# Kernel optimization log

Hardware: AMD Instinct MI355X
Metric: run time of the kernel (lower is better)

Reference implementation:

```python
import jax, jax.numpy as jnp
import numpy as np

B, S, H = 2, 2048, 1024
NUM_HEAD = 16
HEAD = H // NUM_HEAD
NEG = -10000000000.0


def setup_inputs() -> dict:
    key = jax.random.key(0)
    ks = jax.random.split(key, 10)
    scale = 1.0 / np.sqrt(H)
    return {
        "query": jax.random.normal(ks[0], (B, S, H), jnp.float32),
        "key": jax.random.normal(ks[1], (B, S, H), jnp.float32),
        "value": jax.random.normal(ks[2], (B, S, H), jnp.float32),
        "mask": jax.random.randint(ks[3], (B, S), 0, 2, jnp.int32),
        "Wq": jax.random.normal(ks[4], (H, H), jnp.float32) * scale,
        "bq": jnp.zeros((H,), jnp.float32),
        "Wk": jax.random.normal(ks[5], (H, H), jnp.float32) * scale,
        "bk": jnp.zeros((H,), jnp.float32),
        "Wv": jax.random.normal(ks[6], (H, H), jnp.float32) * scale,
        "bv": jnp.zeros((H,), jnp.float32),
    }


def reference(query, key, value, mask, Wq, bq, Wk, bk, Wv, bv):
    b, s, h = query.shape
    # Linear projections (torch Linear: x @ W.T + b), split into heads -> [b, nh, s, hd]
    def proj(x, W, bias):
        y = x @ W.T + bias
        return y.reshape(b, s, NUM_HEAD, HEAD).transpose(0, 2, 1, 3)

    q = proj(query, Wq, bq)
    k = proj(key, Wk, bk)
    v = proj(value, Wv, bv)

    # NOTE: original module has NO 1/sqrt(head_dim) scaling -- faithful.
    attn_score = jnp.einsum("bhqd,bhkd->bhqk", q, k)  # [b, nh, s, s]
    # key-padding mask bias: 0 where mask==1, -1e10 where mask==0, broadcast over query dim
    bias_add = jnp.where(mask[:, None, None, :] == 0, NEG, 0.0).astype(attn_score.dtype)
    attn_score = attn_score + bias_add
    attn_ratio = jax.nn.softmax(attn_score, axis=-1)
    out = jnp.einsum("bhqk,bhkd->bhqd", attn_ratio, v)  # [b, nh, s, hd]
    out = out.transpose(0, 2, 1, 3).reshape(b, s, h)
    # Dropout is identity in eval mode; output_linear is defined but never used in forward.
    return out
```

## Files before the change

### kernel.cpp

```cpp
#include <hip/hip_runtime.h>

#define BATCH 2
#define S_LEN 2048
#define HDIM  1024
#define NHEAD 16
#define HD    64
#define NEGBIAS -1e10f

typedef __attribute__((ext_vector_type(8))) _Float16 half8;
typedef __attribute__((ext_vector_type(4))) _Float16 half4;
typedef __attribute__((ext_vector_type(4))) float   f32x4;

__global__ __launch_bounds__(256) void cvt_w(
    const float* __restrict__ Wq, const float* __restrict__ Wk,
    const float* __restrict__ Wv, _Float16* __restrict__ Wf)
{
    const int z = blockIdx.y;
    const float* src = (z == 0) ? Wq : (z == 1) ? Wk : Wv;
    _Float16* dst = Wf + (size_t)z * (HDIM * HDIM);
    size_t i = ((size_t)blockIdx.x * 256 + threadIdx.x) * 8;
    float4 a0 = *(const float4*)(src + i);
    float4 a1 = *(const float4*)(src + i + 4);
    half8 v;
    v[0] = (_Float16)a0.x; v[1] = (_Float16)a0.y;
    v[2] = (_Float16)a0.z; v[3] = (_Float16)a0.w;
    v[4] = (_Float16)a1.x; v[5] = (_Float16)a1.y;
    v[6] = (_Float16)a1.z; v[7] = (_Float16)a1.w;
    *(half8*)(dst + i) = v;
}

__global__ __launch_bounds__(256) void proj_gemm_f16(
    const float* __restrict__ Xq, const float* __restrict__ Xk,
    const float* __restrict__ Xv, const _Float16* __restrict__ Wf,
    const float* __restrict__ bq, const float* __restrict__ bk,
    const float* __restrict__ bv,
    _Float16* __restrict__ Qb, _Float16* __restrict__ Kb, _Float16* __restrict__ Vtb)
{
    const int z = blockIdx.z;
    const float* X    = (z == 0) ? Xq : (z == 1) ? Xk : Xv;
    const float* bias = (z == 0) ? bq : (z == 1) ? bk : bv;
    const _Float16* Wz = Wf + (size_t)z * (HDIM * HDIM);
    _Float16* Y       = (z == 0) ? Qb : (z == 1) ? Kb : Vtb;

    const int n0 = blockIdx.x * 128;
    const int m0 = blockIdx.y * 128;

    __shared__ __align__(16) _Float16 As[128][40];
    __shared__ __align__(16) _Float16 Bs[128][40];

    const int t    = threadIdx.x;
    const int w    = t >> 6;
    const int lane = t & 63;
    const int quad = lane >> 4;
    const int lc   = lane & 15;
    const int wm   = (w >> 1) * 64;
    const int wn   = (w & 1) * 64;

    const f32x4 fzero = {0.f, 0.f, 0.f, 0.f};
    f32x4 acc[4][4];
#pragma unroll
    for (int i = 0; i < 4; i++)
#pragma unroll
        for (int j = 0; j < 4; j++) acc[i][j] = fzero;

    const int srow = t >> 2;
    const int sc   = t & 3;

    for (int k0 = 0; k0 < HDIM; k0 += 32) {
#pragma unroll
        for (int half = 0; half < 2; half++) {
            int row = srow + half * 64;
            {
                const float* g = X + (size_t)(m0 + row) * HDIM + k0 + sc * 8;
                float4 a0 = *(const float4*)g;
                float4 a1 = *(const float4*)(g + 4);
                half8 v;
                v[0] = (_Float16)a0.x; v[1] = (_Float16)a0.y;
                v[2] = (_Float16)a0.z; v[3] = (_Float16)a0.w;
                v[4] = (_Float16)a1.x; v[5] = (_Float16)a1.y;
                v[6] = (_Float16)a1.z; v[7] = (_Float16)a1.w;
                *(half8*)&As[row][sc * 8] = v;
            }
            *(half8*)&Bs[row][sc * 8] =
                *(const half8*)(Wz + (size_t)(n0 + row) * HDIM + k0 + sc * 8);
        }
        __syncthreads();

        half8 af[4], bf[4];
#pragma unroll
        for (int mt = 0; mt < 4; mt++)
            af[mt] = *(const half8*)&As[wm + mt * 16 + lc][quad * 8];
#pragma unroll
        for (int nt = 0; nt < 4; nt++)
            bf[nt] = *(const half8*)&Bs[wn + nt * 16 + lc][quad * 8];
#pragma unroll
        for (int mt = 0; mt < 4; mt++)
#pragma unroll
            for (int nt = 0; nt < 4; nt++)
                acc[mt][nt] = __builtin_amdgcn_mfma_f32_16x16x32_f16(
                    af[mt], bf[nt], acc[mt][nt], 0, 0, 0);
        __syncthreads();
    }

#pragma unroll
    for (int nt = 0; nt < 4; nt++) {
        const int n = n0 + wn + nt * 16 + lc;
        const float bv_ = bias[n];
        const int h = n >> 6, d = n & 63;
#pragma unroll
        for (int mt = 0; mt < 4; mt++) {
#pragma unroll
            for (int r = 0; r < 4; r++) {
                const int m = m0 + wm + mt * 16 + quad * 4 + r;
                const int b = m >> 11, s = m & (S_LEN - 1);
                const int bh = b * NHEAD + h;
                _Float16 val = (_Float16)(acc[mt][nt][r] + bv_);
                if (z == 2)
                    Y[((size_t)bh * HD + d) * S_LEN + s] = val;
                else
                    Y[((size_t)bh * S_LEN + s) * HD + d] = val;
            }
        }
    }
}

__global__ __launch_bounds__(256) void flash_attn_mfma(
    const _Float16* __restrict__ Qb, const _Float16* __restrict__ Kb,
    const _Float16* __restrict__ Vtb, const int* __restrict__ mask,
    float* __restrict__ out)
{
    const int qt = blockIdx.x & 15;
    const int bh = blockIdx.x >> 4;
    const int b  = bh >> 4;
    const int h  = bh & (NHEAD - 1);

    __shared__ __align__(16) _Float16 Ks [64][72];
    __shared__ __align__(16) _Float16 Vts[64][72];
    __shared__ __align__(16) _Float16 Ps [4][32][72];
    __shared__ float biasS[64];

    const int t    = threadIdx.x;
    const int w    = t >> 6;
    const int lane = t & 63;
    const int quad = lane >> 4;
    const int lc   = lane & 15;

    const _Float16* Kbase = Kb  + (size_t)bh * S_LEN * HD;
    const _Float16* Vbase = Vtb + (size_t)bh * HD * S_LEN;

    half8 qf[2][2];
#pragma unroll
    for (int qg = 0; qg < 2; qg++) {
        const int qrow = qt * 128 + w * 32 + qg * 16 + lc;
#pragma unroll
        for (int s = 0; s < 2; s++)
            qf[qg][s] = *(const half8*)(Qb + ((size_t)bh * S_LEN + qrow) * HD
                                        + s * 32 + quad * 8);
    }

    const f32x4 fzero = {0.f, 0.f, 0.f, 0.f};
    f32x4 o[2][4];
#pragma unroll
    for (int qg = 0; qg < 2; qg++)
#pragma unroll
        for (int nt = 0; nt < 4; nt++) o[qg][nt] = fzero;
    float mrun[2] = {-3.0e38f, -3.0e38f};
    float lrun[2] = {0.f, 0.f};

    for (int kt = 0; kt < S_LEN; kt += 64) {
#pragma unroll
        for (int i = 0; i < 2; i++) {
            int c  = t + 256 * i;
            int rr = c >> 3;
            int cc = (c & 7) * 8;
            *(half8*)&Ks[rr][cc] =
                *(const half8*)(Kbase + (size_t)(kt + rr) * HD + cc);
            *(half8*)&Vts[rr][cc] =
                *(const half8*)(Vbase + (size_t)rr * S_LEN + kt + cc);
        }
        if (t < 64) biasS[t] = mask[b * S_LEN + kt + t] ? 0.f : NEGBIAS;
        __syncthreads();

        f32x4 scf[2][4];
#pragma unroll
        for (int qg = 0; qg < 2; qg++)
#pragma unroll
            for (int tt = 0; tt < 4; tt++) scf[qg][tt] = fzero;
#pragma unroll
        for (int s = 0; s < 2; s++) {
#pragma unroll
            for (int tt = 0; tt < 4; tt++) {
                half8 kf = *(const half8*)&Ks[tt * 16 + lc][s * 32 + quad * 8];
                scf[0][tt] = __builtin_amdgcn_mfma_f32_16x16x32_f16(kf, qf[0][s], scf[0][tt], 0, 0, 0);
                scf[1][tt] = __builtin_amdgcn_mfma_f32_16x16x32_f16(kf, qf[1][s], scf[1][tt], 0, 0, 0);
            }
        }

#pragma unroll
        for (int tt = 0; tt < 4; tt++) {
            float4 b4 = *(const float4*)&biasS[tt * 16 + quad * 4];
#pragma unroll
            for (int qg = 0; qg < 2; qg++) {
                scf[qg][tt][0] += b4.x; scf[qg][tt][1] += b4.y;
                scf[qg][tt][2] += b4.z; scf[qg][tt][3] += b4.w;
            }
        }

#pragma unroll
        for (int qg = 0; qg < 2; qg++) {
            float mx = scf[qg][0][0];
#pragma unroll
            for (int tt = 0; tt < 4; tt++)
#pragma unroll
                for (int r = 0; r < 4; r++) mx = fmaxf(mx, scf[qg][tt][r]);
            mx = fmaxf(mx, __shfl_xor(mx, 16));
            mx = fmaxf(mx, __shfl_xor(mx, 32));

            float mn = fmaxf(mrun[qg], mx);
            float al = __expf(mrun[qg] - mn);
            float ls = 0.f;
#pragma unroll
            for (int tt = 0; tt < 4; tt++)
#pragma unroll
                for (int r = 0; r < 4; r++) {
                    float p = __expf(scf[qg][tt][r] - mn);
                    scf[qg][tt][r] = p;
                    ls += p;
                }
            ls += __shfl_xor(ls, 16);
            ls += __shfl_xor(ls, 32);
            lrun[qg] = lrun[qg] * al + ls;
            mrun[qg] = mn;
#pragma unroll
            for (int nt = 0; nt < 4; nt++) {
                o[qg][nt][0] *= al; o[qg][nt][1] *= al;
                o[qg][nt][2] *= al; o[qg][nt][3] *= al;
            }

#pragma unroll
            for (int tt = 0; tt < 4; tt++) {
                half4 pk;
                pk[0] = (_Float16)scf[qg][tt][0]; pk[1] = (_Float16)scf[qg][tt][1];
                pk[2] = (_Float16)scf[qg][tt][2]; pk[3] = (_Float16)scf[qg][tt][3];
                *(half4*)&Ps[w][qg * 16 + lc][tt * 16 + quad * 4] = pk;
            }
        }

#pragma unroll
        for (int s = 0; s < 2; s++) {
            half8 pf0 = *(const half8*)&Ps[w][lc]     [s * 32 + quad * 8];
            half8 pf1 = *(const half8*)&Ps[w][16 + lc][s * 32 + quad * 8];
#pragma unroll
            for (int nt = 0; nt < 4; nt++) {
                half8 vf = *(const half8*)&Vts[nt * 16 + lc][s * 32 + quad * 8];
                o[0][nt] = __builtin_amdgcn_mfma_f32_16x16x32_f16(vf, pf0, o[0][nt], 0, 0, 0);
                o[1][nt] = __builtin_amdgcn_mfma_f32_16x16x32_f16(vf, pf1, o[1][nt], 0, 0, 0);
            }
        }
        __syncthreads();
    }

#pragma unroll
    for (int qg = 0; qg < 2; qg++) {
        const int qrow = qt * 128 + w * 32 + qg * 16 + lc;
        const float inv = 1.f / lrun[qg];
        const size_t rowb = ((size_t)b * S_LEN + qrow) * HDIM + h * HD;
#pragma unroll
        for (int nt = 0; nt < 4; nt++) {
            float4 v;
            v.x = o[qg][nt][0] * inv; v.y = o[qg][nt][1] * inv;
            v.z = o[qg][nt][2] * inv; v.w = o[qg][nt][3] * inv;
            *(float4*)&out[rowb + nt * 16 + quad * 4] = v;
        }
    }
}

extern "C" void kernel_launch(void* const* d_in, const int* in_sizes, int n_in,
                              void* d_out, int out_size, void* d_ws, size_t ws_size,
                              hipStream_t stream) {
    const float* query = (const float*)d_in[0];
    const float* key   = (const float*)d_in[1];
    const float* value = (const float*)d_in[2];
    const int*   mask  = (const int*)  d_in[3];
    const float* Wq    = (const float*)d_in[4];
    const float* bq    = (const float*)d_in[5];
    const float* Wk    = (const float*)d_in[6];
    const float* bk    = (const float*)d_in[7];
    const float* Wv    = (const float*)d_in[8];
    const float* bv    = (const float*)d_in[9];
    float* out = (float*)d_out;

    const size_t nElem = (size_t)BATCH * S_LEN * HDIM;
    const size_t wElem = (size_t)HDIM * HDIM;
    if (ws_size < (3 * nElem + 3 * wElem) * sizeof(_Float16)) return;
    _Float16* Qb  = (_Float16*)d_ws;
    _Float16* Kb  = Qb + nElem;
    _Float16* Vtb = Kb + nElem;
    _Float16* Wf  = Vtb + nElem;

    dim3 gcvt(wElem / (256 * 8), 3);
    cvt_w<<<gcvt, 256, 0, stream>>>(Wq, Wk, Wv, Wf);

    dim3 gproj(HDIM / 128, (BATCH * S_LEN) / 128, 3);
    proj_gemm_f16<<<gproj, 256, 0, stream>>>(query, key, value, Wf,
                                             bq, bk, bv, Qb, Kb, Vtb);

    flash_attn_mfma<<<BATCH * NHEAD * (S_LEN / 128), 256, 0, stream>>>(
        Qb, Kb, Vtb, mask, out);
}
```

Before: 246.6 us.

## Split attention over two key halves and merge with a combine kernel

Attention blocks now process only half of the key sequence each, doubling the grid, and write unnormalized fp16 partial outputs plus running max and sum. A new combine kernel rescales the two partials with log-sum-exp weights and writes the normalized fp32 output. This aims to raise occupancy and parallelism across CUs. It costs extra global traffic for the partials, an extra launch, and fp16 rounding of unnormalized accumulators.

```diff
diff --git a/kernel.cpp b/kernel.cpp
--- a/kernel.cpp
+++ b/kernel.cpp
@@ -6,6 +6,7 @@
 #define NHEAD 16
 #define HD    64
 #define NEGBIAS -1e10f
+#define NQE   (BATCH * NHEAD * S_LEN)
 
 typedef __attribute__((ext_vector_type(8))) _Float16 half8;
 typedef __attribute__((ext_vector_type(4))) _Float16 half4;
@@ -124,15 +125,17 @@
     }
 }
 
-__global__ __launch_bounds__(256) void flash_attn_mfma(
+__global__ __launch_bounds__(256) void flash_attn_split(
     const _Float16* __restrict__ Qb, const _Float16* __restrict__ Kb,
     const _Float16* __restrict__ Vtb, const int* __restrict__ mask,
-    float* __restrict__ out)
+    _Float16* __restrict__ Opart, float* __restrict__ Mpart,
+    float* __restrict__ Lpart)
 {
-    const int qt = blockIdx.x & 15;
-    const int bh = blockIdx.x >> 4;
-    const int b  = bh >> 4;
-    const int h  = bh & (NHEAD - 1);
+    const int qt   = blockIdx.x & 15;
+    const int bh   = blockIdx.x >> 4;
+    const int half = blockIdx.y;
+    const int b    = bh >> 4;
+    const int koff = half * (S_LEN / 2);
 
     __shared__ __align__(16) _Float16 Ks [64][72];
     __shared__ __align__(16) _Float16 Vts[64][72];
@@ -167,18 +170,18 @@
     float mrun[2] = {-3.0e38f, -3.0e38f};
     float lrun[2] = {0.f, 0.f};
 
-    for (int kt = 0; kt < S_LEN; kt += 64) {
+    for (int kt = 0; kt < S_LEN / 2; kt += 64) {
 #pragma unroll
         for (int i = 0; i < 2; i++) {
             int c  = t + 256 * i;
             int rr = c >> 3;
             int cc = (c & 7) * 8;
             *(half8*)&Ks[rr][cc] =
-                *(const half8*)(Kbase + (size_t)(kt + rr) * HD + cc);
+                *(const half8*)(Kbase + (size_t)(koff + kt + rr) * HD + cc);
             *(half8*)&Vts[rr][cc] =
-                *(const half8*)(Vbase + (size_t)rr * S_LEN + kt + cc);
-        }
-        if (t < 64) biasS[t] = mask[b * S_LEN + kt + t] ? 0.f : NEGBIAS;
+                *(const half8*)(Vbase + (size_t)rr * S_LEN + koff + kt + cc);
+        }
+        if (t < 64) biasS[t] = mask[b * S_LEN + koff + kt + t] ? 0.f : NEGBIAS;
         __syncthreads();
 
         f32x4 scf[2][4];
@@ -263,16 +266,51 @@
 #pragma unroll
     for (int qg = 0; qg < 2; qg++) {
         const int qrow = qt * 128 + w * 32 + qg * 16 + lc;
-        const float inv = 1.f / lrun[qg];
-        const size_t rowb = ((size_t)b * S_LEN + qrow) * HDIM + h * HD;
+        const size_t qe = (size_t)half * NQE + (size_t)bh * S_LEN + qrow;
+        if (quad == 0) { Mpart[qe] = mrun[qg]; Lpart[qe] = lrun[qg]; }
 #pragma unroll
         for (int nt = 0; nt < 4; nt++) {
-            float4 v;
-            v.x = o[qg][nt][0] * inv; v.y = o[qg][nt][1] * inv;
-            v.z = o[qg][nt][2] * inv; v.w = o[qg][nt][3] * inv;
-            *(float4*)&out[rowb + nt * 16 + quad * 4] = v;
-        }
-    }
+            half4 pk;
+            pk[0] = (_Float16)o[qg][nt][0]; pk[1] = (_Float16)o[qg][nt][1];
+            pk[2] = (_Float16)o[qg][nt][2]; pk[3] = (_Float16)o[qg][nt][3];
+            *(half4*)&Opart[qe * HD + nt * 16 + quad * 4] = pk;
+        }
+    }
+}
+
+__global__ __launch_bounds__(256) void combine_halves(
+    const _Float16* __restrict__ Opart, const float* __restrict__ Mpart,
+    const float* __restrict__ Lpart, float* __restrict__ out)
+{
+    const int idx = blockIdx.x * 256 + threadIdx.x;
+    const int dg  = idx & 7;
+    const int qe  = idx >> 3;
+    const int bh  = qe >> 11;
+    const int q   = qe & (S_LEN - 1);
+    const int b   = bh >> 4;
+    const int h   = bh & (NHEAD - 1);
+
+    const float m1 = Mpart[qe],       l1 = Lpart[qe];
+    const float m2 = Mpart[NQE + qe], l2 = Lpart[NQE + qe];
+    const float M  = fmaxf(m1, m2);
+    const float w1 = __expf(m1 - M), w2 = __expf(m2 - M);
+    const float inv = 1.f / (w1 * l1 + w2 * l2);
+
+    half8 o1 = *(const half8*)&Opart[(size_t)qe * HD + dg * 8];
+    half8 o2 = *(const half8*)&Opart[(size_t)NQE * HD + (size_t)qe * HD + dg * 8];
+
+    float* dst = out + ((size_t)b * S_LEN + q) * HDIM + h * HD + dg * 8;
+    float4 r0, r1;
+    r0.x = (w1 * (float)o1[0] + w2 * (float)o2[0]) * inv;
+    r0.y = (w1 * (float)o1[1] + w2 * (float)o2[1]) * inv;
+    r0.z = (w1 * (float)o1[2] + w2 * (float)o2[2]) * inv;
+    r0.w = (w1 * (float)o1[3] + w2 * (float)o2[3]) * inv;
+    r1.x = (w1 * (float)o1[4] + w2 * (float)o2[4]) * inv;
+    r1.y = (w1 * (float)o1[5] + w2 * (float)o2[5]) * inv;
+    r1.z = (w1 * (float)o1[6] + w2 * (float)o2[6]) * inv;
+    r1.w = (w1 * (float)o1[7] + w2 * (float)o2[7]) * inv;
+    *(float4*)dst = r0;
+    *(float4*)(dst + 4) = r1;
 }
 
 extern "C" void kernel_launch(void* const* d_in, const int* in_sizes, int n_in,
@@ -292,11 +330,16 @@
 
     const size_t nElem = (size_t)BATCH * S_LEN * HDIM;
     const size_t wElem = (size_t)HDIM * HDIM;
-    if (ws_size < (3 * nElem + 3 * wElem) * sizeof(_Float16)) return;
-    _Float16* Qb  = (_Float16*)d_ws;
-    _Float16* Kb  = Qb + nElem;
-    _Float16* Vtb = Kb + nElem;
-    _Float16* Wf  = Vtb + nElem;
+    const size_t need = (3 * nElem + 3 * wElem + 2 * nElem) * sizeof(_Float16)
+                      + 4 * (size_t)NQE * sizeof(float);
+    if (ws_size < need) return;
+    _Float16* Qb    = (_Float16*)d_ws;
+    _Float16* Kb    = Qb + nElem;
+    _Float16* Vtb   = Kb + nElem;
+    _Float16* Wf    = Vtb + nElem;
+    _Float16* Opart = Wf + 3 * wElem;
+    float*    Mpart = (float*)(Opart + 2 * nElem);
+    float*    Lpart = Mpart + 2 * NQE;
 
     dim3 gcvt(wElem / (256 * 8), 3);
     cvt_w<<<gcvt, 256, 0, stream>>>(Wq, Wk, Wv, Wf);
@@ -305,6 +348,9 @@
     proj_gemm_f16<<<gproj, 256, 0, stream>>>(query, key, value, Wf,
                                              bq, bk, bv, Qb, Kb, Vtb);
 
-    flash_attn_mfma<<<BATCH * NHEAD * (S_LEN / 128), 256, 0, stream>>>(
-        Qb, Kb, Vtb, mask, out);
-}
+    dim3 gattn(BATCH * NHEAD * (S_LEN / 128), 2);
+    flash_attn_split<<<gattn, 256, 0, stream>>>(Qb, Kb, Vtb, mask,
+                                                Opart, Mpart, Lpart);
+
+    combine_halves<<<(NQE * 8) / 256, 256, 0, stream>>>(Opart, Mpart, Lpart, out);
+}
```

After: 266.0 us. +7.9%, slower.

## Register-prefetch next tiles in projection and attention loops; drop weight conversion kernel

Applied to the files above, without the earlier changes.

Both the projection GEMM and the flash-attention loop now load the next K-step tile from global memory into registers before computing on the current shared-memory tile. This hides global latency behind MFMA work, and the trailing barrier is replaced by one at the top of the next iteration. The separate fp32-to-fp16 weight conversion kernel is removed; weights are read as fp32 and converted inline in the GEMM, saving a launch at the cost of twice the weight read bytes per tile. Register pressure rises from holding the prefetched tiles, which may lower occupancy.

```diff
diff --git a/kernel.cpp b/kernel.cpp
--- a/kernel.cpp
+++ b/kernel.cpp
@@ -11,35 +11,16 @@
 typedef __attribute__((ext_vector_type(4))) _Float16 half4;
 typedef __attribute__((ext_vector_type(4))) float   f32x4;
 
-__global__ __launch_bounds__(256) void cvt_w(
-    const float* __restrict__ Wq, const float* __restrict__ Wk,
-    const float* __restrict__ Wv, _Float16* __restrict__ Wf)
-{
-    const int z = blockIdx.y;
-    const float* src = (z == 0) ? Wq : (z == 1) ? Wk : Wv;
-    _Float16* dst = Wf + (size_t)z * (HDIM * HDIM);
-    size_t i = ((size_t)blockIdx.x * 256 + threadIdx.x) * 8;
-    float4 a0 = *(const float4*)(src + i);
-    float4 a1 = *(const float4*)(src + i + 4);
-    half8 v;
-    v[0] = (_Float16)a0.x; v[1] = (_Float16)a0.y;
-    v[2] = (_Float16)a0.z; v[3] = (_Float16)a0.w;
-    v[4] = (_Float16)a1.x; v[5] = (_Float16)a1.y;
-    v[6] = (_Float16)a1.z; v[7] = (_Float16)a1.w;
-    *(half8*)(dst + i) = v;
-}
-
 __global__ __launch_bounds__(256) void proj_gemm_f16(
-    const float* __restrict__ Xq, const float* __restrict__ Xk,
-    const float* __restrict__ Xv, const _Float16* __restrict__ Wf,
-    const float* __restrict__ bq, const float* __restrict__ bk,
-    const float* __restrict__ bv,
+    const float* __restrict__ Xq, const float* __restrict__ Wq, const float* __restrict__ bq,
+    const float* __restrict__ Xk, const float* __restrict__ Wk, const float* __restrict__ bk,
+    const float* __restrict__ Xv, const float* __restrict__ Wv, const float* __restrict__ bv,
     _Float16* __restrict__ Qb, _Float16* __restrict__ Kb, _Float16* __restrict__ Vtb)
 {
     const int z = blockIdx.z;
     const float* X    = (z == 0) ? Xq : (z == 1) ? Xk : Xv;
+    const float* W    = (z == 0) ? Wq : (z == 1) ? Wk : Wv;
     const float* bias = (z == 0) ? bq : (z == 1) ? bk : bv;
-    const _Float16* Wz = Wf + (size_t)z * (HDIM * HDIM);
     _Float16* Y       = (z == 0) ? Qb : (z == 1) ? Kb : Vtb;
 
     const int n0 = blockIdx.x * 128;
@@ -66,25 +47,43 @@
     const int srow = t >> 2;
     const int sc   = t & 3;
 
+    float4 xa[2][2], wa[2][2];
+#define PROJ_ISSUE(K0)                                                        \
+    {                                                                         \
+        _Pragma("unroll")                                                     \
+        for (int hf = 0; hf < 2; hf++) {                                      \
+            const float* gx = X + (size_t)(m0 + srow + hf * 64) * HDIM + (K0) + sc * 8; \
+            xa[hf][0] = *(const float4*)gx;                                   \
+            xa[hf][1] = *(const float4*)(gx + 4);                             \
+            const float* gw = W + (size_t)(n0 + srow + hf * 64) * HDIM + (K0) + sc * 8; \
+            wa[hf][0] = *(const float4*)gw;                                   \
+            wa[hf][1] = *(const float4*)(gw + 4);                             \
+        }                                                                     \
+    }
+
+    PROJ_ISSUE(0)
+
     for (int k0 = 0; k0 < HDIM; k0 += 32) {
-#pragma unroll
-        for (int half = 0; half < 2; half++) {
-            int row = srow + half * 64;
-            {
-                const float* g = X + (size_t)(m0 + row) * HDIM + k0 + sc * 8;
-                float4 a0 = *(const float4*)g;
-                float4 a1 = *(const float4*)(g + 4);
-                half8 v;
-                v[0] = (_Float16)a0.x; v[1] = (_Float16)a0.y;
-                v[2] = (_Float16)a0.z; v[3] = (_Float16)a0.w;
-                v[4] = (_Float16)a1.x; v[5] = (_Float16)a1.y;
-                v[6] = (_Float16)a1.z; v[7] = (_Float16)a1.w;
-                *(half8*)&As[row][sc * 8] = v;
-            }
-            *(half8*)&Bs[row][sc * 8] =
-                *(const half8*)(Wz + (size_t)(n0 + row) * HDIM + k0 + sc * 8);
+        if (k0) __syncthreads();
+#pragma unroll
+        for (int hf = 0; hf < 2; hf++) {
+            int row = srow + hf * 64;
+            half8 vx;
+            vx[0] = (_Float16)xa[hf][0].x; vx[1] = (_Float16)xa[hf][0].y;
+            vx[2] = (_Float16)xa[hf][0].z; vx[3] = (_Float16)xa[hf][0].w;
+            vx[4] = (_Float16)xa[hf][1].x; vx[5] = (_Float16)xa[hf][1].y;
+            vx[6] = (_Float16)xa[hf][1].z; vx[7] = (_Float16)xa[hf][1].w;
+            *(half8*)&As[row][sc * 8] = vx;
+            half8 vw;
+            vw[0] = (_Float16)wa[hf][0].x; vw[1] = (_Float16)wa[hf][0].y;
+            vw[2] = (_Float16)wa[hf][0].z; vw[3] = (_Float16)wa[hf][0].w;
+            vw[4] = (_Float16)wa[hf][1].x; vw[5] = (_Float16)wa[hf][1].y;
+            vw[6] = (_Float16)wa[hf][1].z; vw[7] = (_Float16)wa[hf][1].w;
+            *(half8*)&Bs[row][sc * 8] = vw;
         }
         __syncthreads();
+
+        if (k0 + 32 < HDIM) PROJ_ISSUE(k0 + 32)
 
         half8 af[4], bf[4];
 #pragma unroll
@@ -99,7 +98,6 @@
             for (int nt = 0; nt < 4; nt++)
                 acc[mt][nt] = __builtin_amdgcn_mfma_f32_16x16x32_f16(
                     af[mt], bf[nt], acc[mt][nt], 0, 0, 0);
-        __syncthreads();
     }
 
 #pragma unroll
@@ -147,6 +145,7 @@
 
     const _Float16* Kbase = Kb  + (size_t)bh * S_LEN * HD;
     const _Float16* Vbase = Vtb + (size_t)bh * HD * S_LEN;
+    const int* mbase = mask + b * S_LEN;
 
     half8 qf[2][2];
 #pragma unroll
@@ -167,19 +166,32 @@
     float mrun[2] = {-3.0e38f, -3.0e38f};
     float lrun[2] = {0.f, 0.f};
 
+    const int rr0 = t >> 3,          cc0 = (t & 7) * 8;
+    const int rr1 = (t + 256) >> 3,  cc1 = (t & 7) * 8;
+
+    half8 kpre[2], vpre[2];
+    int   mpre;
+#define ATTN_ISSUE(KT)                                                        \
+    {                                                                         \
+        kpre[0] = *(const half8*)(Kbase + (size_t)((KT) + rr0) * HD + cc0);   \
+        kpre[1] = *(const half8*)(Kbase + (size_t)((KT) + rr1) * HD + cc1);   \
+        vpre[0] = *(const half8*)(Vbase + (size_t)rr0 * S_LEN + (KT) + cc0);  \
+        vpre[1] = *(const half8*)(Vbase + (size_t)rr1 * S_LEN + (KT) + cc1);  \
+        mpre    = mbase[(KT) + (t & 63)];                                     \
+    }
+
+    ATTN_ISSUE(0)
+
     for (int kt = 0; kt < S_LEN; kt += 64) {
-#pragma unroll
-        for (int i = 0; i < 2; i++) {
-            int c  = t + 256 * i;
-            int rr = c >> 3;
-            int cc = (c & 7) * 8;
-            *(half8*)&Ks[rr][cc] =
-                *(const half8*)(Kbase + (size_t)(kt + rr) * HD + cc);
-            *(half8*)&Vts[rr][cc] =
-                *(const half8*)(Vbase + (size_t)rr * S_LEN + kt + cc);
-        }
-        if (t < 64) biasS[t] = mask[b * S_LEN + kt + t] ? 0.f : NEGBIAS;
+        if (kt) __syncthreads();
+        *(half8*)&Ks [rr0][cc0] = kpre[0];
+        *(half8*)&Ks [rr1][cc1] = kpre[1];
+        *(half8*)&Vts[rr0][cc0] = vpre[0];
+        *(half8*)&Vts[rr1][cc1] = vpre[1];
+        if (t < 64) biasS[t] = mpre ? 0.f : NEGBIAS;
         __syncthreads();
+
+        if (kt + 64 < S_LEN) ATTN_ISSUE(kt + 64)
 
         f32x4 scf[2][4];
 #pragma unroll
@@ -257,7 +269,6 @@
                 o[1][nt] = __builtin_amdgcn_mfma_f32_16x16x32_f16(vf, pf1, o[1][nt], 0, 0, 0);
             }
         }
-        __syncthreads();
     }
 
 #pragma unroll
@@ -291,19 +302,14 @@
     float* out = (float*)d_out;
 
     const size_t nElem = (size_t)BATCH * S_LEN * HDIM;
-    const size_t wElem = (size_t)HDIM * HDIM;
-    if (ws_size < (3 * nElem + 3 * wElem) * sizeof(_Float16)) return;
+    if (ws_size < 3 * nElem * sizeof(_Float16)) return;
     _Float16* Qb  = (_Float16*)d_ws;
     _Float16* Kb  = Qb + nElem;
     _Float16* Vtb = Kb + nElem;
-    _Float16* Wf  = Vtb + nElem;
-
-    dim3 gcvt(wElem / (256 * 8), 3);
-    cvt_w<<<gcvt, 256, 0, stream>>>(Wq, Wk, Wv, Wf);
 
     dim3 gproj(HDIM / 128, (BATCH * S_LEN) / 128, 3);
-    proj_gemm_f16<<<gproj, 256, 0, stream>>>(query, key, value, Wf,
-                                             bq, bk, bv, Qb, Kb, Vtb);
+    proj_gemm_f16<<<gproj, 256, 0, stream>>>(query, Wq, bq, key, Wk, bk,
+                                             value, Wv, bv, Qb, Kb, Vtb);
 
     flash_attn_mfma<<<BATCH * NHEAD * (S_LEN / 128), 256, 0, stream>>>(
         Qb, Kb, Vtb, mask, out);
```

New measurement: 239.6 us. -2.8%, faster.
